# Kernel optimization log

Hardware: AMD Instinct MI355X
Metric: run time of the kernel (lower is better)

## Reference

```python
import jax, jax.numpy as jnp
import numpy as np

B, S = 4, 1800
DA, DP = 438, 72          # audio feat dim, pose dim
DM, NH, DK, DV = 200, 8, 64, 64
DI = 1024                 # ffn inner dim == decoder LSTM hidden
DE = 200                  # pose_emb_size
NL = 2                    # encoder layers
WIN = 100                 # sliding window size
COND, LAMBDA_V = 10, 0.01


def _sinusoid_table(n_pos, d):
    pos = np.arange(n_pos)[:, None].astype(np.float64)
    i = np.arange(d)[None, :]
    ang = pos / np.power(10000.0, 2 * (i // 2) / d)
    t = np.zeros((n_pos, d))
    t[:, 0::2] = np.sin(ang[:, 0::2])
    t[:, 1::2] = np.cos(ang[:, 1::2])
    t[0] = 0.0  # padding_idx
    return jnp.asarray(t, jnp.float32)


def _layer_norm(x, g, b, eps=1e-5):
    m = x.mean(-1, keepdims=True)
    v = ((x - m) ** 2).mean(-1, keepdims=True)
    return (x - m) * jax.lax.rsqrt(v + eps) * g + b


def _lstm_cell(x, h, c, Wih, Whh, bih, bhh):
    g = x @ Wih + h @ Whh + bih + bhh
    i, f, gg, o = jnp.split(g, 4, axis=-1)  # torch gate order i,f,g,o
    c2 = jax.nn.sigmoid(f) * c + jax.nn.sigmoid(i) * jnp.tanh(gg)
    h2 = jax.nn.sigmoid(o) * jnp.tanh(c2)
    return h2, c2


def setup_inputs() -> dict:
    key = jax.random.key(0)
    ks = iter(jax.random.split(key, 64))
    sc = 0.05
    d = {}
    d['src_seq'] = jax.random.normal(next(ks), (B, S, DA), jnp.float32)
    d['tgt_seq'] = jax.random.normal(next(ks), (B, S, DP), jnp.float32)
    d['bos'] = jax.random.normal(next(ks), (B, DP), jnp.float32)
    d['h_init'] = jax.random.normal(next(ks), (3, B, DI), jnp.float32)
    d['c_init'] = jax.random.normal(next(ks), (3, B, DI), jnp.float32)
    d['epoch_i'] = 100
    d['enc_emb_W'] = jax.random.normal(next(ks), (DA, DM)) * sc
    d['enc_emb_b'] = jnp.zeros((DM,))
    d['Wq'] = jax.random.normal(next(ks), (NL, DM, NH * DK)) * sc
    d['bq'] = jnp.zeros((NL, NH * DK))
    d['Wk'] = jax.random.normal(next(ks), (NL, DM, NH * DK)) * sc
    d['bk'] = jnp.zeros((NL, NH * DK))
    d['Wv'] = jax.random.normal(next(ks), (NL, DM, NH * DV)) * sc
    d['bv'] = jnp.zeros((NL, NH * DV))
    d['Wo'] = jax.random.normal(next(ks), (NL, NH * DV, DM)) * sc
    d['bo'] = jnp.zeros((NL, DM))
    d['ln1_g'] = jnp.ones((NL, DM)); d['ln1_b'] = jnp.zeros((NL, DM))
    d['W1'] = jax.random.normal(next(ks), (NL, DM, DI)) * sc
    d['b1'] = jnp.zeros((NL, DI))
    d['W2'] = jax.random.normal(next(ks), (NL, DI, DM)) * sc
    d['b2'] = jnp.zeros((NL, DM))
    d['ln2_g'] = jnp.ones((NL, DM)); d['ln2_b'] = jnp.zeros((NL, DM))
    d['tgt_W'] = jax.random.normal(next(ks), (DP, DE)) * sc
    d['tgt_b'] = jnp.zeros((DE,))
    d['Wih1'] = jax.random.normal(next(ks), (DE, 4 * DI)) * sc
    d['Whh1'] = jax.random.normal(next(ks), (DI, 4 * DI)) * sc
    d['bih1'] = jnp.zeros((4 * DI,)); d['bhh1'] = jnp.zeros((4 * DI,))
    d['Wih2'] = jax.random.normal(next(ks), (DI, 4 * DI)) * sc
    d['Whh2'] = jax.random.normal(next(ks), (DI, 4 * DI)) * sc
    d['bih2'] = jnp.zeros((4 * DI,)); d['bhh2'] = jnp.zeros((4 * DI,))
    d['Wih3'] = jax.random.normal(next(ks), (DI, 4 * DI)) * sc
    d['Whh3'] = jax.random.normal(next(ks), (DI, 4 * DI)) * sc
    d['bih3'] = jnp.zeros((4 * DI,)); d['bhh3'] = jnp.zeros((4 * DI,))
    d['out_W'] = jax.random.normal(next(ks), (DI + DM, DP)) * sc
    d['out_b'] = jnp.zeros((DP,))
    return d


def _forward(src_seq, tgt_seq, bos, h_init, c_init,
             enc_emb_W, enc_emb_b, Wq, bq, Wk, bk, Wv, bv, Wo, bo,
             ln1_g, ln1_b, W1, b1, W2, b2, ln2_g, ln2_b,
             tgt_W, tgt_b, Wih1, Whh1, bih1, bhh1,
             Wih2, Whh2, bih2, bhh2, Wih3, Whh3, bih3, bhh3,
             out_W, out_b, epoch_i):
    # ---------------- Encoder ----------------
    pos = _sinusoid_table(S + 1, DM)[1:S + 1]          # src_pos = arange(S)+1
    x = src_seq @ enc_emb_W + enc_emb_b + pos[None]    # [B,S,DM]
    r = jnp.arange(S)
    keep = jnp.abs(r[:, None] - r[None, :]) <= WIN     # sliding-window band
    for l in range(NL):
        res = x
        q = (x @ Wq[l] + bq[l]).reshape(B, S, NH, DK)
        k = (x @ Wk[l] + bk[l]).reshape(B, S, NH, DK)
        v = (x @ Wv[l] + bv[l]).reshape(B, S, NH, DV)
        att = jnp.einsum('bihd,bjhd->bhij', q, k) / np.sqrt(DK).astype(np.float32)
        att = jnp.where(keep[None, None], att, -1e9)
        att = jax.nn.softmax(att, axis=-1)
        o = jnp.einsum('bhij,bjhd->bihd', att, v).reshape(B, S, NH * DV)
        x = _layer_norm(o @ Wo[l] + bo[l] + res, ln1_g[l], ln1_b[l])
        x = _layer_norm(jax.nn.relu(x @ W1[l] + b1[l]) @ W2[l] + b2[l] + x,
                        ln2_g[l], ln2_b[l])
    enc = x                                            # [B,S,DM]

    # -------- teacher-forcing mask (epoch_i is a Python int) --------
    p = int(epoch_i * LAMBDA_V)
    m = np.concatenate([np.zeros((S, p)), np.ones((S, COND))], 1).reshape(-1)[:S]
    tf_mask = jnp.asarray(m.astype(bool))

    def step(carry, xs):
        h, c, prev = carry                             # h,c: [3,B,DI]
        tgt_t, enc_t, use_gt = xs
        dec_in = jnp.where(use_gt, tgt_t, jax.lax.stop_gradient(prev))
        e = dec_in @ tgt_W + tgt_b
        h0, c0 = _lstm_cell(e,    h[0], c[0], Wih1, Whh1, bih1, bhh1)
        h1, c1 = _lstm_cell(h[0], h[1], c[1], Wih2, Whh2, bih2, bhh2)  # old h0
        h2, c2 = _lstm_cell(h[1], h[2], c[2], Wih3, Whh3, bih3, bhh3)  # old h1
        out = jnp.concatenate([h2, enc_t], -1) @ out_W + out_b
        return (jnp.stack([h0, h1, h2]), jnp.stack([c0, c1, c2]), out), out

    xs = (tgt_seq.transpose(1, 0, 2), enc.transpose(1, 0, 2), tf_mask)
    _, outs = jax.lax.scan(step, (h_init, c_init, bos), xs)
    return outs.transpose(1, 0, 2)                     # [B,S,DP]


def reference(src_seq, tgt_seq, bos, h_init, c_init,
              enc_emb_W, enc_emb_b, Wq, bq, Wk, bk, Wv, bv, Wo, bo,
              ln1_g, ln1_b, W1, b1, W2, b2, ln2_g, ln2_b,
              tgt_W, tgt_b, Wih1, Whh1, bih1, bhh1,
              Wih2, Whh2, bih2, bhh2, Wih3, Whh3, bih3, bhh3,
              out_W, out_b, epoch_i):
    return _forward(src_seq, tgt_seq, bos, h_init, c_init,
                    enc_emb_W, enc_emb_b, Wq, bq, Wk, bk, Wv, bv, Wo, bo,
                    ln1_g, ln1_b, W1, b1, W2, b2, ln2_g, ln2_b,
                    tgt_W, tgt_b, Wih1, Whh1, bih1, bhh1,
                    Wih2, Whh2, bih2, bhh2, Wih3, Whh3, bih3, bhh3,
                    out_W, out_b, epoch_i)
```

## Files before the change

### kernel.cpp

```cpp
#include <hip/hip_runtime.h>

#define SQ 1800
#define NBLK 256

typedef _Float16 h2v __attribute__((ext_vector_type(2)));
#define AGT __HIP_MEMORY_SCOPE_AGENT

__device__ __forceinline__ float bf2f(unsigned short u){ return __uint_as_float(((unsigned)u)<<16); }
__device__ __forceinline__ unsigned short f2bf(float f){
  unsigned u=__float_as_uint(f);
  unsigned r=u+0x7FFFu+((u>>16)&1u);
  return (unsigned short)(r>>16);
}
__device__ __forceinline__ float sigm(float x){ return 1.0f/(1.0f+__expf(-x)); }
__device__ __forceinline__ unsigned pack16(float a, float b){
  _Float16 ha=(_Float16)a, hb=(_Float16)b;
  unsigned short ua=__builtin_bit_cast(unsigned short,ha), ub=__builtin_bit_cast(unsigned short,hb);
  return (unsigned)ua | ((unsigned)ub<<16);
}
__device__ __forceinline__ float lo16(unsigned v){ h2v h=__builtin_bit_cast(h2v,v); return (float)h[0]; }
__device__ __forceinline__ float hi16(unsigned v){ h2v h=__builtin_bit_cast(h2v,v); return (float)h[1]; }
__device__ __forceinline__ float hdot2(unsigned uw, unsigned ux, float acc){
  h2v a=__builtin_bit_cast(h2v,uw), b=__builtin_bit_cast(h2v,ux);
#if __has_builtin(__builtin_amdgcn_fdot2)
  return __builtin_amdgcn_fdot2(a,b,acc,false);
#else
  return acc + (float)a[0]*(float)b[0] + (float)a[1]*(float)b[1];
#endif
}
__device__ __forceinline__ unsigned aload(const unsigned* p){
  return __hip_atomic_load(p,__ATOMIC_RELAXED,AGT);
}
__device__ __forceinline__ unsigned long long aload64(const unsigned long long* p){
  return __hip_atomic_load(p,__ATOMIC_RELAXED,AGT);
}
__device__ __forceinline__ void astore(unsigned* p, unsigned v){
  __hip_atomic_store(p,v,__ATOMIC_RELAXED,AGT);
}


__global__ __launch_bounds__(256) void k_postab(float* __restrict__ pt){
  int idx=blockIdx.x*256+threadIdx.x; if(idx>=SQ*200) return;
  int t=idx/200, j=idx%200;
  double ang=(double)(t+1)*pow(10000.0, -(double)(2*(j/2))/200.0);
  pt[idx]=(float)((j&1)? cos(ang) : sin(ang));
}

__global__ __launch_bounds__(256) void k_we(const float* __restrict__ tgtW, const float* __restrict__ Wih1, float* __restrict__ We){
  int idx=blockIdx.x*256+threadIdx.x;
  int k=idx>>12, j=idx&4095;
  float acc=0.f;
  for(int m=0;m<200;m++) acc+=tgtW[k*200+m]*Wih1[(size_t)m*4096+j];
  We[idx]=acc;
}

__global__ __launch_bounds__(256) void k_bias(const float* __restrict__ tgtb, const float* __restrict__ Wih1,
    const float* __restrict__ bih1,const float* __restrict__ bhh1,const float* __restrict__ bih2,const float* __restrict__ bhh2,
    const float* __restrict__ bih3,const float* __restrict__ bhh3,float* __restrict__ bias){
  int idx=blockIdx.x*256+threadIdx.x; if(idx>=3*4096) return;
  int l=idx>>12, j=idx&4095;
  float v;
  if(l==0){ v=bih1[j]+bhh1[j]; for(int m=0;m<200;m++) v+=tgtb[m]*Wih1[(size_t)m*4096+j]; }
  else if(l==1) v=bih2[j]+bhh2[j];
  else v=bih3[j]+bhh3[j];
  bias[idx]=v;
}

__global__ __launch_bounds__(256) void k_packf(const float* __restrict__ We, const float* __restrict__ Whh1,
  const float* __restrict__ Wih2, const float* __restrict__ Whh2,
  const float* __restrict__ Wih3, const float* __restrict__ Whh3, unsigned* __restrict__ P){
  size_t idx=(size_t)blockIdx.x*256+threadIdx.x;
  const float *A, *Bm; size_t l; int stride, KA, K;
  if(idx < 2359296u){ l=idx; stride=2304; A=We; Bm=Whh1; KA=72; K=1096; }
  else if(idx < 6684672u){ l=idx-2359296u; stride=4224; A=Wih2; Bm=Whh2; KA=1024; K=2048; }
  else { l=idx-6684672u; stride=4224; A=Wih3; Bm=Whh3; KA=1024; K=2048; }
  int u=(int)(l/(size_t)stride); int r=(int)(l-(size_t)u*stride);
  int k2=r>>2, g=r&3, k=2*k2;
  float w0=0.f,w1=0.f;
  if(k<K){
    int col=g*1024+u;
    w0 = (k   < KA)? A[(size_t)k*4096+col]      : Bm[(size_t)(k-KA)*4096+col];
    w1 = (k+1 < KA)? A[(size_t)(k+1)*4096+col]  : Bm[(size_t)(k+1-KA)*4096+col];
  }
  P[idx]=pack16(w0,w1);
}

__global__ __launch_bounds__(256) void k_outwt(const float* __restrict__ outW, float* __restrict__ outWT){
  int idx=blockIdx.x*256+threadIdx.x; if(idx>=72*1024) return;
  int j=idx>>10, u=idx&1023;
  outWT[idx]=outW[(size_t)u*72+j];
}


__global__ __launch_bounds__(256) void k_embed(const float* __restrict__ src, const float* __restrict__ W,
    const float* __restrict__ bias, const float* __restrict__ posb, float* __restrict__ xout){
  __shared__ float s[8][438];
  int row0=blockIdx.x*8, tid=threadIdx.x;
  for(int idx=tid; idx<8*438; idx+=256){ int r=idx/438,k=idx%438; s[r][k]=src[(size_t)(row0+r)*438+k]; }
  __syncthreads();
  int j=tid; if(j<200){
    float acc[8];
    #pragma unroll
    for(int r=0;r<8;r++){ int t=(row0+r)%SQ; acc[r]=bias[j]+posb[t*200+j]; }
    for(int k=0;k<438;k++){
      float w=W[(size_t)k*200+j];
      #pragma unroll
      for(int r=0;r<8;r++) acc[r]+=s[r][k]*w;
    }
    for(int r=0;r<8;r++) xout[(size_t)(row0+r)*200+j]=acc[r];
  }
}

template<int K,int N,int CPT,bool RELU>
__global__ __launch_bounds__(256) void k_gemm8(const float* __restrict__ A, const float* __restrict__ W,
    const float* __restrict__ bias, float* __restrict__ out){
  __shared__ float s[8][K];
  int row0=blockIdx.x*8, tid=threadIdx.x;
  for(int idx=tid; idx<8*K; idx+=256){ int r=idx/K,k=idx%K; s[r][k]=A[(size_t)(row0+r)*K+k]; }
  __syncthreads();
  int j0=tid*CPT;
  float acc[8][CPT];
  #pragma unroll
  for(int r=0;r<8;r++)
    #pragma unroll
    for(int c=0;c<CPT;c++) acc[r][c]=bias[j0+c];
  for(int k=0;k<K;k++){
    float w[CPT];
    #pragma unroll
    for(int c=0;c<CPT;c++) w[c]=W[(size_t)k*N+j0+c];
    #pragma unroll
    for(int r=0;r<8;r++){ float a=s[r][k];
      #pragma unroll
      for(int c=0;c<CPT;c++) acc[r][c]+=a*w[c];
    }
  }
  #pragma unroll
  for(int r=0;r<8;r++)
    #pragma unroll
    for(int c=0;c<CPT;c++){ float v=acc[r][c]; if(RELU) v=fmaxf(v,0.f); out[(size_t)(row0+r)*N+j0+c]=v; }
}

__global__ __launch_bounds__(256) void k_attn(const float* __restrict__ Q, const float* __restrict__ Km,
    const float* __restrict__ V, float* __restrict__ O){
  int bid=blockIdx.x;
  int it=bid%225; int h=(bid/225)&7; int b=bid/1800;
  int i0=it*8;
  int j0=i0-100; if(j0<0) j0=0;
  int j1=i0+7+101; if(j1>SQ) j1=SQ;
  int JN=j1-j0;
  __shared__ unsigned short kld[208][66];
  __shared__ unsigned short vld[208][66];
  __shared__ float q[8][64];
  __shared__ float sc[8][208];
  int tid=threadIdx.x;
  for(int idx=tid; idx<JN*64; idx+=256){
    int j=idx>>6, d=idx&63;
    size_t src=((size_t)(b*SQ+j0+j)*8+h)*64+d;
    kld[j][d]=f2bf(Km[src]);
    vld[j][d]=f2bf(V[src]);
  }
  for(int idx=tid; idx<8*64; idx+=256){ int r=idx>>6,d=idx&63; q[r][d]=Q[((size_t)(b*SQ+i0+r)*8+h)*64+d]; }
  __syncthreads();
  {
    int r=tid>>5, js=tid&31;
    int i=i0+r;
    for(int j=js;j<JN;j+=32){
      int jg=j0+j; int diff=i-jg; if(diff<0) diff=-diff;
      float s=-1e30f;
      if(diff<=100){
        s=0.f;
        for(int d=0;d<64;d++) s+=q[r][d]*bf2f(kld[j][d]);
        s*=0.125f;
      }
      sc[r][j]=s;
    }
  }
  __syncthreads();
  {
    int wv=tid>>6, lane=tid&63;
    for(int rr=wv*2; rr<wv*2+2; rr++){
      float m=-1e30f;
      for(int j=lane;j<JN;j+=64) m=fmaxf(m,sc[rr][j]);
      for(int o=32;o;o>>=1) m=fmaxf(m,__shfl_xor(m,o));
      float sum=0.f;
      for(int j=lane;j<JN;j+=64){ float e=__expf(sc[rr][j]-m); sc[rr][j]=e; sum+=e; }
      for(int o=32;o;o>>=1) sum+=__shfl_xor(sum,o);
      float inv=1.f/sum;
      for(int j=lane;j<JN;j+=64) sc[rr][j]*=inv;
    }
  }
  __syncthreads();
  {
    int d=tid&63, rb=tid>>6;
    for(int rr=rb; rr<8; rr+=4){
      float acc=0.f;
      for(int j=0;j<JN;j++) acc+=sc[rr][j]*bf2f(vld[j][d]);
      O[((size_t)(b*SQ+i0+rr)*8+h)*64+d]=acc;
    }
  }
}

template<int K>
__global__ __launch_bounds__(256) void k_matln(const float* __restrict__ A, const float* __restrict__ W,
    const float* __restrict__ bias, const float* __restrict__ g, const float* __restrict__ bt, float* __restrict__ x){
  __shared__ float s[8][K];
  __shared__ float y[8][200];
  int row0=blockIdx.x*8, tid=threadIdx.x;
  for(int idx=tid; idx<8*K; idx+=256){ int r=idx/K,k=idx%K; s[r][k]=A[(size_t)(row0+r)*K+k]; }
  __syncthreads();
  if(tid<200){
    int j=tid;
    float acc[8];
    #pragma unroll
    for(int r=0;r<8;r++) acc[r]=bias[j];
    for(int k=0;k<K;k++){
      float w=W[(size_t)k*200+j];
      #pragma unroll
      for(int r=0;r<8;r++) acc[r]+=s[r][k]*w;
    }
    #pragma unroll
    for(int r=0;r<8;r++) y[r][j]=acc[r]+x[(size_t)(row0+r)*200+j];
  }
  __syncthreads();
  int wv=tid>>6, lane=tid&63;
  for(int rr=wv*2; rr<wv*2+2; rr++){
    float sm=0.f,s2=0.f;
    for(int j=lane;j<200;j+=64){ float v=y[rr][j]; sm+=v; s2+=v*v; }
    for(int o=32;o;o>>=1){ sm+=__shfl_xor(sm,o); s2+=__shfl_xor(s2,o); }
    float mean=sm*(1.f/200.f);
    float var=s2*(1.f/200.f)-mean*mean;
    float inv=rsqrtf(var+1e-5f);
    for(int j=lane;j<200;j+=64) x[(size_t)(row0+rr)*200+j]=(y[rr][j]-mean)*inv*g[j]+bt[j];
  }
}

__global__ __launch_bounds__(320) void k_encpart(const float* __restrict__ x, const float* __restrict__ outW,
    const float* __restrict__ outb, float* __restrict__ ep){
  int t=blockIdx.x, tid=threadIdx.x;
  __shared__ float el[4][200];
  for(int idx=tid; idx<800; idx+=320){ int b=idx/200,k=idx%200; el[b][k]=x[((size_t)b*SQ+t)*200+k]; }
  __syncthreads();
  if(tid<288){
    int b=tid/72, j=tid%72;
    float acc=outb[j];
    for(int k=0;k<200;k++) acc+=el[b][k]*outW[(size_t)(1024+k)*72+j];
    ep[((size_t)b*SQ+t)*72+j]=acc;
  }
}


__device__ __forceinline__ void gridbar(unsigned* bar, unsigned gen){
  __syncthreads();
  if(threadIdx.x==0){
    int g=blockIdx.x>>4;
    unsigned r=__hip_atomic_fetch_add(&bar[g*32],1u,__ATOMIC_RELAXED,AGT);
    if(r==gen*16u+15u){
      unsigned rt=__hip_atomic_fetch_add(&bar[16*32],1u,__ATOMIC_RELAXED,AGT);
      if(rt==gen*16u+15u){
        __hip_atomic_store(&bar[17*32],gen+1u,__ATOMIC_RELAXED,AGT);
      }
    }
    unsigned f;
    do{ __builtin_amdgcn_s_sleep(1);
        f=__hip_atomic_load(&bar[17*32],__ATOMIC_RELAXED,AGT);
    }while(f<gen+1u);
  }
  __syncthreads();
}

__global__ __launch_bounds__(512,2) void k_dec(
  const uint4* __restrict__ P4, const float* __restrict__ bias,
  unsigned* __restrict__ hbufU, unsigned* __restrict__ fbbufU,
  unsigned* __restrict__ h2allU, unsigned* __restrict__ bar,
  const float* __restrict__ tgt, const float* __restrict__ bos,
  const float* __restrict__ h_init, const float* __restrict__ c_init,
  const float* __restrict__ encp, const float* __restrict__ outWT)
{
  __shared__ __align__(16) unsigned xs2[2688*4];
  __shared__ float red[16*513];
  __shared__ float gsum[192];
  __shared__ float c_lds[48];
  __shared__ float htmp[48];
  __shared__ float ldspad[1200];
  int tid=threadIdx.x, blk=blockIdx.x;
  if(tid==0) ldspad[0]=0.f;

  int uu, ks;
  if(tid<128){ uu=tid>>5; ks=tid&31; }
  else if(tid<320){ int l=tid-128; uu=4+l/48; ks=l-(uu-4)*48; }
  else { int l=tid-320; uu=8+l/48; ks=l-(uu-8)*48; }
  int cell = uu<4?0:(uu<8?1:2);
  int u_loc=uu&3, u_glob=blk*4+u_loc;
  size_t ubase4 = (cell==0)? (size_t)u_glob*576 :
                  (cell==1)? (589824u + (size_t)u_glob*1056) :
                             (1671168u + (size_t)u_glob*1056);
  int xoff = (cell==0)?0:(cell==1?576:1632);

  uint4 w[22];
  if(tid<128){
    #pragma unroll
    for(int i=0;i<18;i++) w[i]=P4[ubase4 + (size_t)ks + (size_t)i*32];
  } else {
    #pragma unroll
    for(int i=0;i<22;i++) w[i]=P4[ubase4 + (size_t)ks + (size_t)i*48];
  }

  int dty[6], dlp[6];
  #pragma unroll
  for(int q=0;q<6;q++){
    int r=tid+512*q; dty[q]=2; dlp[q]=0;
    if(r<2688){
      int cl, rr;
      if(r<576){cl=0;rr=r;} else if(r<1632){cl=1;rr=r-576;} else {cl=2;rr=r-1632;}
      if(cl==0){
        if(rr<36){ dty[q]=1; dlp[q]=2*rr; }
        else if(rr<548){ dty[q]=0; dlp[q]=(0*512+(rr-36))*2; }
      } else {
        int l0=(cl==1)?0:1;
        if(rr<512){ dty[q]=0; dlp[q]=(l0*512+rr)*2; }
        else if(rr<1024){ dty[q]=0; dlp[q]=((l0+1)*512+(rr-512))*2; }
      }
    }
  }

  if(tid<48){
    int uu0=tid>>2, b0=tid&3;
    int cl=uu0<4?0:(uu0<8?1:2);
    c_lds[tid]=c_init[((size_t)cl*4+b0)*1024 + (size_t)blk*4+(uu0&3)];
  }
  __syncthreads();

  const unsigned long long* hb64=(const unsigned long long*)hbufU;
  unsigned gen=0;
  for(int t=0;t<SQ;t++){
    bool fb=(t>0)&&(t%11==0);
    if(fb){
      if(blk<72 && tid<256){
        int j=blk, b=tid>>6, lane=tid&63, pv=(t-1)&1;
        float s=0.f;
        #pragma unroll
        for(int q=0;q<8;q++){
          int u2=lane+q*64;
          unsigned v=aload(&hbufU[(size_t)(((pv*3+2)*512)+u2)*4+b]);
          s += lo16(v)*outWT[(size_t)j*1024+2*u2] + hi16(v)*outWT[(size_t)j*1024+2*u2+1];
        }
        #pragma unroll
        for(int o=32;o;o>>=1) s+=__shfl_xor(s,o);
        if(lane==0) astore(&fbbufU[b*72+j], __float_as_uint(s + encp[((size_t)b*SQ+(t-1))*72+j]));
      }
      gridbar(bar,gen); gen++;
    }

    if(t==0){
      #pragma unroll
      for(int q=0;q<6;q++){
        if(q==5 && tid>=128) break;
        uint4 vv={0u,0u,0u,0u};
        if(dty[q]==1){
          int j=dlp[q];
          const float2 f0=*(const float2*)&bos[0*72+j];
          const float2 f1=*(const float2*)&bos[1*72+j];
          const float2 f2=*(const float2*)&bos[2*72+j];
          const float2 f3=*(const float2*)&bos[3*72+j];
          vv.x=pack16(f0.x,f0.y); vv.y=pack16(f1.x,f1.y);
          vv.z=pack16(f2.x,f2.y); vv.w=pack16(f3.x,f3.y);
        } else if(dty[q]==0){
          int lp=dlp[q]>>10, pr=(dlp[q]>>1)&511;
          const float2 f0=*(const float2*)&h_init[((size_t)lp*4+0)*1024+2*pr];
          const float2 f1=*(const float2*)&h_init[((size_t)lp*4+1)*1024+2*pr];
          const float2 f2=*(const float2*)&h_init[((size_t)lp*4+2)*1024+2*pr];
          const float2 f3=*(const float2*)&h_init[((size_t)lp*4+3)*1024+2*pr];
          vv.x=pack16(f0.x,f0.y); vv.y=pack16(f1.x,f1.y);
          vv.z=pack16(f2.x,f2.y); vv.w=pack16(f3.x,f3.y);
        }
        *(uint4*)&xs2[(size_t)(tid+512*q)*4]=vv;
      }
    } else {
      size_t pvoff=(size_t)(((t-1)&1)*3*512*2);
      #pragma unroll
      for(int q=0;q<6;q++){
        if(q==5 && tid>=128) break;
        int ty=dty[q];
        if(ty==0){
          unsigned long long a=aload64(hb64+pvoff+dlp[q]);
          unsigned long long c=aload64(hb64+pvoff+dlp[q]+1);
          uint4 vv; vv.x=(unsigned)a; vv.y=(unsigned)(a>>32);
          vv.z=(unsigned)c; vv.w=(unsigned)(c>>32);
          *(uint4*)&xs2[(size_t)(tid+512*q)*4]=vv;
        } else if(ty==1){
          int j=dlp[q];
          uint4 vv;
          if(fb){
            vv.x=pack16(__uint_as_float(aload(&fbbufU[0*72+j])),__uint_as_float(aload(&fbbufU[0*72+j+1])));
            vv.y=pack16(__uint_as_float(aload(&fbbufU[1*72+j])),__uint_as_float(aload(&fbbufU[1*72+j+1])));
            vv.z=pack16(__uint_as_float(aload(&fbbufU[2*72+j])),__uint_as_float(aload(&fbbufU[2*72+j+1])));
            vv.w=pack16(__uint_as_float(aload(&fbbufU[3*72+j])),__uint_as_float(aload(&fbbufU[3*72+j+1])));
          } else {
            const float2 f0=*(const float2*)&tgt[((size_t)0*SQ+t)*72+j];
            const float2 f1=*(const float2*)&tgt[((size_t)1*SQ+t)*72+j];
            const float2 f2=*(const float2*)&tgt[((size_t)2*SQ+t)*72+j];
            const float2 f3=*(const float2*)&tgt[((size_t)3*SQ+t)*72+j];
            vv.x=pack16(f0.x,f0.y); vv.y=pack16(f1.x,f1.y);
            vv.z=pack16(f2.x,f2.y); vv.w=pack16(f3.x,f3.y);
          }
          *(uint4*)&xs2[(size_t)(tid+512*q)*4]=vv;
        }
      }
    }
    __syncthreads();

    {
      float acc[16];
      #pragma unroll
      for(int a=0;a<16;a++) acc[a]=0.f;
      auto run=[&](int NIT,int NKS){
        #pragma unroll
        for(int i=0;i<22;i++){
          if(i>=NIT) break;
          const uint4 xv=*(const uint4*)&xs2[(size_t)(xoff+ks+i*NKS)*4];
          const unsigned* wu=(const unsigned*)&w[i];
          const unsigned* xu=(const unsigned*)&xv;
          #pragma unroll
          for(int g=0;g<4;g++)
            #pragma unroll
            for(int b=0;b<4;b++)
              acc[g*4+b]=hdot2(wu[g],xu[b],acc[g*4+b]);
        }
      };
      if(tid<128) run(18,32); else run(22,48);
      #pragma unroll
      for(int a=0;a<16;a++) red[a*513+tid]=acc[a];
    }
    __syncthreads();

    if(tid<192){
      int uuo=tid>>4, a=tid&15;
      int base,n;
      if(uuo<4){base=uuo*32;n=32;} else {base=128+(uuo-4)*48;n=48;}
      float s=0.f;
      for(int j2=0;j2<n;j2++) s+=red[a*513+base+j2];
      int cl=uuo<4?0:(uuo<8?1:2), g=a>>2;
      gsum[tid]=s+bias[(size_t)cl*4096+(size_t)g*1024+blk*4+(uuo&3)];
    }
    __syncthreads();

    if(tid<48){
      int uup=tid>>2,b=tid&3;
      float gi=gsum[uup*16+b],gf=gsum[uup*16+4+b],gg=gsum[uup*16+8+b],go=gsum[uup*16+12+b];
      float cp=c_lds[tid];
      float cn=sigm(gf)*cp+sigm(gi)*tanhf(gg);
      float hn=sigm(go)*tanhf(cn);
      c_lds[tid]=cn; htmp[tid]=hn;
    }
    __syncthreads();
    if(tid<48 && !(tid&4)){
      int uup=tid>>2,b=tid&3;
      int cl=uup<4?0:(uup<8?1:2), ul=uup&3;
      unsigned v=pack16(htmp[tid],htmp[tid+4]);
      int pr=blk*2+(ul>>1);
      astore(&hbufU[(size_t)(((t&1)*3+cl)*512+pr)*4+b], v);
      if(cl==2) astore(&h2allU[((size_t)t*4+b)*512+pr], v);
    }
    gridbar(bar,gen); gen++;
  }
}

__global__ __launch_bounds__(320) void k_out(const unsigned* __restrict__ h2allU, const float* __restrict__ outW,
    const float* __restrict__ enc_part, float* __restrict__ out){
  int t=blockIdx.x, tid=threadIdx.x;
  __shared__ float h2l[4][1024];
  for(int idx=tid; idx<2048; idx+=320){
    int b=idx>>9, p=idx&511;
    unsigned v=h2allU[((size_t)t*4+b)*512+p];
    h2l[b][2*p]=lo16(v); h2l[b][2*p+1]=hi16(v);
  }
  __syncthreads();
  if(tid<288){
    int b=tid/72, j=tid%72;
    float acc=enc_part[((size_t)b*SQ+t)*72+j];
    for(int u=0;u<1024;u++) acc+=h2l[b][u]*outW[(size_t)u*72+j];
    out[((size_t)b*SQ+t)*72+j]=acc;
  }
}

extern "C" void kernel_launch(void* const* d_in, const int* in_sizes, int n_in,
                              void* d_out, int out_size, void* d_ws, size_t ws_size,
                              hipStream_t stream) {
  (void)in_sizes; (void)n_in; (void)out_size; (void)ws_size;
  const float* src   =(const float*)d_in[0];
  const float* tgt   =(const float*)d_in[1];
  const float* bos   =(const float*)d_in[2];
  const float* h_init=(const float*)d_in[3];
  const float* c_init=(const float*)d_in[4];
  const float* eW    =(const float*)d_in[6];
  const float* eb    =(const float*)d_in[7];
  const float* Wq    =(const float*)d_in[8];
  const float* bq    =(const float*)d_in[9];
  const float* Wk    =(const float*)d_in[10];
  const float* bk    =(const float*)d_in[11];
  const float* Wv    =(const float*)d_in[12];
  const float* bv    =(const float*)d_in[13];
  const float* Wo    =(const float*)d_in[14];
  const float* bo    =(const float*)d_in[15];
  const float* ln1g  =(const float*)d_in[16];
  const float* ln1b  =(const float*)d_in[17];
  const float* W1    =(const float*)d_in[18];
  const float* b1    =(const float*)d_in[19];
  const float* W2    =(const float*)d_in[20];
  const float* b2    =(const float*)d_in[21];
  const float* ln2g  =(const float*)d_in[22];
  const float* ln2b  =(const float*)d_in[23];
  const float* tgtW  =(const float*)d_in[24];
  const float* tgtb  =(const float*)d_in[25];
  const float* Wih1  =(const float*)d_in[26];
  const float* Whh1  =(const float*)d_in[27];
  const float* bih1  =(const float*)d_in[28];
  const float* bhh1  =(const float*)d_in[29];
  const float* Wih2  =(const float*)d_in[30];
  const float* Whh2  =(const float*)d_in[31];
  const float* bih2  =(const float*)d_in[32];
  const float* bhh2  =(const float*)d_in[33];
  const float* Wih3  =(const float*)d_in[34];
  const float* Whh3  =(const float*)d_in[35];
  const float* bih3  =(const float*)d_in[36];
  const float* bhh3  =(const float*)d_in[37];
  const float* outW  =(const float*)d_in[38];
  const float* outb  =(const float*)d_in[39];
  float* out=(float*)d_out;

  char* wsb=(char*)d_ws; size_t off=0;
  auto alloc=[&](size_t bytes)->void*{ void* p=wsb+off; off+=(bytes+255)&~(size_t)255; return p; };
  unsigned* Pf   =(unsigned*)alloc((size_t)11010048*4);
  float* We   =(float*)alloc((size_t)72*4096*4);
  float* bias =(float*)alloc((size_t)3*4096*4);
  float* outWT=(float*)alloc((size_t)72*1024*4);
  unsigned* hbufU =(unsigned*)alloc((size_t)2*3*512*4*4);
  unsigned* fbbufU=(unsigned*)alloc((size_t)4*72*4);
  unsigned* bar   =(unsigned*)alloc(4096);
  float* encp =(float*)alloc((size_t)7200*72*4);
  float* posb =(float*)alloc((size_t)SQ*200*4);
  float* xb   =(float*)alloc((size_t)7200*200*4);
  float* qb   =(float*)alloc((size_t)7200*512*4);
  float* kb   =(float*)alloc((size_t)7200*512*4);
  float* vb   =(float*)alloc((size_t)7200*512*4);
  float* ob   =(float*)alloc((size_t)7200*512*4);
  unsigned* h2allU=(unsigned*)qb;
  float* mid  =vb;
  (void)kb; (void)ob;

  k_postab<<<(SQ*200+255)/256,256,0,stream>>>(posb);
  k_we<<<72*4096/256,256,0,stream>>>(tgtW,Wih1,We);
  k_bias<<<48,256,0,stream>>>(tgtb,Wih1,bih1,bhh1,bih2,bhh2,bih3,bhh3,bias);
  k_packf<<<43008,256,0,stream>>>(We,Whh1,Wih2,Whh2,Wih3,Whh3,Pf);
  k_outwt<<<(72*1024+255)/256,256,0,stream>>>(outW,outWT);

  k_embed<<<900,256,0,stream>>>(src,eW,eb,posb,xb);
  for(int l=0;l<2;l++){
    k_gemm8<200,512,2,false><<<900,256,0,stream>>>(xb,Wq+(size_t)l*200*512,bq+l*512,qb);
    k_gemm8<200,512,2,false><<<900,256,0,stream>>>(xb,Wk+(size_t)l*200*512,bk+l*512,kb);
    k_gemm8<200,512,2,false><<<900,256,0,stream>>>(xb,Wv+(size_t)l*200*512,bv+l*512,vb);
    k_attn<<<7200,256,0,stream>>>(qb,kb,vb,ob);
    k_matln<512><<<900,256,0,stream>>>(ob,Wo+(size_t)l*512*200,bo+l*200,ln1g+l*200,ln1b+l*200,xb);
    k_gemm8<200,1024,4,true><<<900,256,0,stream>>>(xb,W1+(size_t)l*200*1024,b1+l*1024,mid);
    k_matln<1024><<<900,256,0,stream>>>(mid,W2+(size_t)l*1024*200,b2+l*200,ln2g+l*200,ln2b+l*200,xb);
  }
  k_encpart<<<SQ,320,0,stream>>>(xb,outW,outb,encp);

  hipMemsetAsync(bar,0,4096,stream);
  k_dec<<<NBLK,512,0,stream>>>((const uint4*)Pf,bias,hbufU,fbbufU,h2allU,bar,
                               tgt,bos,h_init,c_init,encp,outWT);

  k_out<<<SQ,320,0,stream>>>(h2allU,outW,encp,out);
}
```

Measured before the change: 14.74 ms.

## Split decoder LSTM into two pipelined block groups with point-to-point flags

The persistent decoder kernel is split into two groups of 128 blocks. Group A computes LSTM layers 1 and 2 and group B computes layer 3, so layer 3 of step t can overlap with layers 1 and 2 of the next step. The single all-block grid barrier is replaced by per-group barriers plus cross-group progress counters, and the hidden-state ring buffer grows from 2 to 4 slots to allow the lag. Weight packing strides change to match the new per-thread k-split. The risk is more complex synchronisation and a possible imbalance between the two groups.

```diff
diff --git a/kernel.cpp b/kernel.cpp
--- a/kernel.cpp
+++ b/kernel.cpp
@@ -72,8 +72,8 @@
   size_t idx=(size_t)blockIdx.x*256+threadIdx.x;
   const float *A, *Bm; size_t l; int stride, KA, K;
   if(idx < 2359296u){ l=idx; stride=2304; A=We; Bm=Whh1; KA=72; K=1096; }
-  else if(idx < 6684672u){ l=idx-2359296u; stride=4224; A=Wih2; Bm=Whh2; KA=1024; K=2048; }
-  else { l=idx-6684672u; stride=4224; A=Wih3; Bm=Whh3; KA=1024; K=2048; }
+  else if(idx < 6782976u){ l=idx-2359296u; stride=4320; A=Wih2; Bm=Whh2; KA=1024; K=2048; }
+  else { l=idx-6782976u; stride=4352; A=Wih3; Bm=Whh3; KA=1024; K=2048; }
   int u=(int)(l/(size_t)stride); int r=(int)(l-(size_t)u*stride);
   int k2=r>>2, g=r&3, k=2*k2;
   float w0=0.f,w1=0.f;
@@ -249,25 +249,6 @@
 }
 
 
-__device__ __forceinline__ void gridbar(unsigned* bar, unsigned gen){
-  __syncthreads();
-  if(threadIdx.x==0){
-    int g=blockIdx.x>>4;
-    unsigned r=__hip_atomic_fetch_add(&bar[g*32],1u,__ATOMIC_RELAXED,AGT);
-    if(r==gen*16u+15u){
-      unsigned rt=__hip_atomic_fetch_add(&bar[16*32],1u,__ATOMIC_RELAXED,AGT);
-      if(rt==gen*16u+15u){
-        __hip_atomic_store(&bar[17*32],gen+1u,__ATOMIC_RELAXED,AGT);
-      }
-    }
-    unsigned f;
-    do{ __builtin_amdgcn_s_sleep(1);
-        f=__hip_atomic_load(&bar[17*32],__ATOMIC_RELAXED,AGT);
-    }while(f<gen+1u);
-  }
-  __syncthreads();
-}
-
 __global__ __launch_bounds__(512,2) void k_dec(
   const uint4* __restrict__ P4, const float* __restrict__ bias,
   unsigned* __restrict__ hbufU, unsigned* __restrict__ fbbufU,
@@ -276,87 +257,93 @@
   const float* __restrict__ h_init, const float* __restrict__ c_init,
   const float* __restrict__ encp, const float* __restrict__ outWT)
 {
-  __shared__ __align__(16) unsigned xs2[2688*4];
+  __shared__ __align__(16) unsigned xs2[1116*4];
   __shared__ float red[16*513];
-  __shared__ float gsum[192];
-  __shared__ float c_lds[48];
-  __shared__ float htmp[48];
-  __shared__ float ldspad[1200];
+  __shared__ float gsum[256];
+  __shared__ float c_lds[64];
+  __shared__ float htmp[64];
+  __shared__ float ldspad[8192];
   int tid=threadIdx.x, blk=blockIdx.x;
+  bool isA = blk<128;
+  int lblk = isA? blk : blk-128;
   if(tid==0) ldspad[0]=0.f;
 
-  int uu, ks;
-  if(tid<128){ uu=tid>>5; ks=tid&31; }
-  else if(tid<320){ int l=tid-128; uu=4+l/48; ks=l-(uu-4)*48; }
-  else { int l=tid-320; uu=8+l/48; ks=l-(uu-8)*48; }
-  int cell = uu<4?0:(uu<8?1:2);
-  int u_loc=uu&3, u_glob=blk*4+u_loc;
-  size_t ubase4 = (cell==0)? (size_t)u_glob*576 :
-                  (cell==1)? (589824u + (size_t)u_glob*1056) :
-                             (1671168u + (size_t)u_glob*1056);
-  int xoff = (cell==0)?0:(cell==1?576:1632);
-
-  uint4 w[22];
-  if(tid<128){
-    #pragma unroll
-    for(int i=0;i<18;i++) w[i]=P4[ubase4 + (size_t)ks + (size_t)i*32];
-  } else {
-    #pragma unroll
-    for(int i=0;i<22;i++) w[i]=P4[ubase4 + (size_t)ks + (size_t)i*48];
-  }
-
-  int dty[6], dlp[6];
+  int slot,ks,NKS,NIT,xoff,cell;
+  if(isA){
+    if(tid<192){ slot=tid/24; ks=tid-slot*24; NKS=24; NIT=24; xoff=0; cell=0; }
+    else { int l=tid-192; slot=8+l/40; ks=l-(slot-8)*40; NKS=40; NIT=27; xoff=36; cell=1; }
+  } else { slot=tid>>6; ks=tid&63; NKS=64; NIT=17; xoff=0; cell=2; }
+  int unit = lblk*8 + (slot&7);
+  size_t ubase4 = (cell==0)? (size_t)unit*576 :
+                  (cell==1)? (589824u + (size_t)unit*1080) :
+                             (1695744u + (size_t)unit*1088);
+
+  uint4 w[27];
   #pragma unroll
-  for(int q=0;q<6;q++){
-    int r=tid+512*q; dty[q]=2; dlp[q]=0;
-    if(r<2688){
-      int cl, rr;
-      if(r<576){cl=0;rr=r;} else if(r<1632){cl=1;rr=r-576;} else {cl=2;rr=r-1632;}
-      if(cl==0){
-        if(rr<36){ dty[q]=1; dlp[q]=2*rr; }
-        else if(rr<548){ dty[q]=0; dlp[q]=(0*512+(rr-36))*2; }
-      } else {
-        int l0=(cl==1)?0:1;
-        if(rr<512){ dty[q]=0; dlp[q]=(l0*512+rr)*2; }
-        else if(rr<1024){ dty[q]=0; dlp[q]=((l0+1)*512+(rr-512))*2; }
-      }
-    }
-  }
-
-  if(tid<48){
-    int uu0=tid>>2, b0=tid&3;
-    int cl=uu0<4?0:(uu0<8?1:2);
-    c_lds[tid]=c_init[((size_t)cl*4+b0)*1024 + (size_t)blk*4+(uu0&3)];
-  }
+  for(int i=0;i<27;i++){ if(i<NIT) w[i]=P4[ubase4 + (size_t)ks + (size_t)i*NKS]; }
+
+  int dty[3], dlp[3];
+  #pragma unroll
+  for(int q=0;q<3;q++){
+    int r=tid+512*q; dty[q]=3; dlp[q]=0;
+    if(isA){
+      if(r<36){ dty[q]=1; dlp[q]=2*r; }
+      else if(r<548){ dty[q]=0; dlp[q]=(r-36)*2; }
+      else if(r<1060){ dty[q]=0; dlp[q]=(512+(r-548))*2; }
+      else if(r<1116){ dty[q]=2; }
+    } else {
+      if(r<512){ dty[q]=0; dlp[q]=(512+r)*2; }
+      else if(r<1024){ dty[q]=0; dlp[q]=(1024+(r-512))*2; }
+      else if(r<1088){ dty[q]=2; }
+    }
+  }
+
+  if(isA){ if(tid<64){ int s=tid>>2,b=tid&3; int cl=(s<8)?0:1;
+           c_lds[tid]=c_init[((size_t)cl*4+b)*1024 + lblk*8+(s&7)]; } }
+  else   { if(tid<32){ int s=tid>>2,b=tid&3;
+           c_lds[tid]=c_init[((size_t)2*4+b)*1024 + lblk*8+s]; } }
   __syncthreads();
 
   const unsigned long long* hb64=(const unsigned long long*)hbufU;
   unsigned gen=0;
   for(int t=0;t<SQ;t++){
     bool fb=(t>0)&&(t%11==0);
-    if(fb){
-      if(blk<72 && tid<256){
-        int j=blk, b=tid>>6, lane=tid&63, pv=(t-1)&1;
+
+    if(!isA && fb){
+      if(lblk<72 && tid<256){
+        int j=lblk, b=tid>>6, lane=tid&63, sl=(t-1)&3;
         float s=0.f;
         #pragma unroll
         for(int q=0;q<8;q++){
           int u2=lane+q*64;
-          unsigned v=aload(&hbufU[(size_t)(((pv*3+2)*512)+u2)*4+b]);
+          unsigned v=aload(&hbufU[(size_t)((sl*3+2)*512+u2)*4+b]);
           s += lo16(v)*outWT[(size_t)j*1024+2*u2] + hi16(v)*outWT[(size_t)j*1024+2*u2+1];
         }
         #pragma unroll
         for(int o=32;o;o>>=1) s+=__shfl_xor(s,o);
         if(lane==0) astore(&fbbufU[b*72+j], __float_as_uint(s + encp[((size_t)b*SQ+(t-1))*72+j]));
       }
-      gridbar(bar,gen); gen++;
+      __syncthreads();
+      if(tid==0 && lblk<72) __hip_atomic_fetch_add(&bar[640],1u,__ATOMIC_RELAXED,AGT);
+    }
+
+    if(isA){
+      if(tid<64){
+        if(t>=2){ while((int)aload(&bar[608]) < t-2) __builtin_amdgcn_s_sleep(1); }
+        if(fb){ unsigned tc=72u*(unsigned)(t/11);
+                while(aload(&bar[640]) < tc) __builtin_amdgcn_s_sleep(1); }
+      }
+    } else if(t>0){
+      if(tid<64){ while((int)aload(&bar[576]) < t) __builtin_amdgcn_s_sleep(1); }
+      __syncthreads();
     }
 
     if(t==0){
       #pragma unroll
-      for(int q=0;q<6;q++){
-        if(q==5 && tid>=128) break;
+      for(int q=0;q<3;q++){
+        int ty=dty[q]; if(ty==3) continue;
         uint4 vv={0u,0u,0u,0u};
-        if(dty[q]==1){
+        if(ty==1){
           int j=dlp[q];
           const float2 f0=*(const float2*)&bos[0*72+j];
           const float2 f1=*(const float2*)&bos[1*72+j];
@@ -364,8 +351,8 @@
           const float2 f3=*(const float2*)&bos[3*72+j];
           vv.x=pack16(f0.x,f0.y); vv.y=pack16(f1.x,f1.y);
           vv.z=pack16(f2.x,f2.y); vv.w=pack16(f3.x,f3.y);
-        } else if(dty[q]==0){
-          int lp=dlp[q]>>10, pr=(dlp[q]>>1)&511;
+        } else if(ty==0){
+          int lp=dlp[q]>>10, pr=(dlp[q]&1023)>>1;
           const float2 f0=*(const float2*)&h_init[((size_t)lp*4+0)*1024+2*pr];
           const float2 f1=*(const float2*)&h_init[((size_t)lp*4+1)*1024+2*pr];
           const float2 f2=*(const float2*)&h_init[((size_t)lp*4+2)*1024+2*pr];
@@ -376,20 +363,18 @@
         *(uint4*)&xs2[(size_t)(tid+512*q)*4]=vv;
       }
     } else {
-      size_t pvoff=(size_t)(((t-1)&1)*3*512*2);
-      #pragma unroll
-      for(int q=0;q<6;q++){
-        if(q==5 && tid>=128) break;
-        int ty=dty[q];
+      size_t pvoff=(size_t)(((t-1)&3)*3*512*2);
+      #pragma unroll
+      for(int q=0;q<3;q++){
+        int ty=dty[q]; if(ty>=2) continue;
+        uint4 vv;
         if(ty==0){
           unsigned long long a=aload64(hb64+pvoff+dlp[q]);
           unsigned long long c=aload64(hb64+pvoff+dlp[q]+1);
-          uint4 vv; vv.x=(unsigned)a; vv.y=(unsigned)(a>>32);
+          vv.x=(unsigned)a; vv.y=(unsigned)(a>>32);
           vv.z=(unsigned)c; vv.w=(unsigned)(c>>32);
-          *(uint4*)&xs2[(size_t)(tid+512*q)*4]=vv;
-        } else if(ty==1){
+        } else {
           int j=dlp[q];
-          uint4 vv;
           if(fb){
             vv.x=pack16(__uint_as_float(aload(&fbbufU[0*72+j])),__uint_as_float(aload(&fbbufU[0*72+j+1])));
             vv.y=pack16(__uint_as_float(aload(&fbbufU[1*72+j])),__uint_as_float(aload(&fbbufU[1*72+j+1])));
@@ -403,8 +388,8 @@
             vv.x=pack16(f0.x,f0.y); vv.y=pack16(f1.x,f1.y);
             vv.z=pack16(f2.x,f2.y); vv.w=pack16(f3.x,f3.y);
           }
-          *(uint4*)&xs2[(size_t)(tid+512*q)*4]=vv;
         }
+        *(uint4*)&xs2[(size_t)(tid+512*q)*4]=vv;
       }
     }
     __syncthreads();
@@ -413,55 +398,90 @@
       float acc[16];
       #pragma unroll
       for(int a=0;a<16;a++) acc[a]=0.f;
-      auto run=[&](int NIT,int NKS){
+      #pragma unroll
+      for(int i=0;i<27;i++){
+        if(i>=NIT) break;
+        const uint4 xv=*(const uint4*)&xs2[(size_t)(xoff+ks+i*NKS)*4];
+        const unsigned* wu=(const unsigned*)&w[i];
+        const unsigned* xu=(const unsigned*)&xv;
         #pragma unroll
-        for(int i=0;i<22;i++){
-          if(i>=NIT) break;
-          const uint4 xv=*(const uint4*)&xs2[(size_t)(xoff+ks+i*NKS)*4];
-          const unsigned* wu=(const unsigned*)&w[i];
-          const unsigned* xu=(const unsigned*)&xv;
+        for(int g=0;g<4;g++)
           #pragma unroll
-          for(int g=0;g<4;g++)
-            #pragma unroll
-            for(int b=0;b<4;b++)
-              acc[g*4+b]=hdot2(wu[g],xu[b],acc[g*4+b]);
+          for(int b=0;b<4;b++)
+            acc[g*4+b]=hdot2(wu[g],xu[b],acc[g*4+b]);
+      }
+      #pragma unroll
+      for(int a=0;a<16;a++) red[a*513+tid]=acc[a];
+    }
+    __syncthreads();
+
+    if(isA){
+      if(tid<256){
+        int s=tid>>4, a=tid&15;
+        int base = (s<8)? s*24 : 192+(s-8)*40;
+        int n = (s<8)? 24 : 40;
+        float sum=0.f;
+        for(int j2=0;j2<n;j2++) sum+=red[a*513+base+j2];
+        int cl=(s<8)?0:1;
+        gsum[tid]=sum+bias[(size_t)cl*4096+(size_t)(a>>2)*1024 + lblk*8+(s&7)];
+      }
+    } else {
+      if(tid<128){
+        int s=tid>>4, a=tid&15;
+        float sum=0.f;
+        for(int j2=0;j2<64;j2++) sum+=red[a*513+s*64+j2];
+        gsum[tid]=sum+bias[(size_t)2*4096+(size_t)(a>>2)*1024 + lblk*8+s];
+      }
+    }
+    __syncthreads();
+
+    if(isA){
+      if(tid<64){
+        int s=tid>>2,b=tid&3;
+        float gi=gsum[s*16+b],gf=gsum[s*16+4+b],gg=gsum[s*16+8+b],go=gsum[s*16+12+b];
+        float cp=c_lds[tid];
+        float cn=sigm(gf)*cp+sigm(gi)*tanhf(gg);
+        float hn=sigm(go)*tanhf(cn);
+        c_lds[tid]=cn; htmp[tid]=hn;
+        if(!(tid&4)){
+          unsigned v=pack16(htmp[tid],htmp[tid+4]);
+          int layer=s>>3, sl=s&7;
+          int pr=lblk*4+(sl>>1);
+          astore(&hbufU[(size_t)(((t&3)*3+layer)*512+pr)*4+b], v);
         }
-      };
-      if(tid<128) run(18,32); else run(22,48);
-      #pragma unroll
-      for(int a=0;a<16;a++) red[a*513+tid]=acc[a];
-    }
+      }
+    } else {
+      if(tid<32){
+        int s=tid>>2,b=tid&3;
+        float gi=gsum[s*16+b],gf=gsum[s*16+4+b],gg=gsum[s*16+8+b],go=gsum[s*16+12+b];
+        float cp=c_lds[tid];
+        float cn=sigm(gf)*cp+sigm(gi)*tanhf(gg);
+        float hn=sigm(go)*tanhf(cn);
+        c_lds[tid]=cn; htmp[tid]=hn;
+        if(!(tid&4)){
+          unsigned v=pack16(htmp[tid],htmp[tid+4]);
+          int pr=lblk*4+(s>>1);
+          astore(&hbufU[(size_t)(((t&3)*3+2)*512+pr)*4+b], v);
+          astore(&h2allU[((size_t)t*4+b)*512+pr], v);
+        }
+      }
+    }
+
     __syncthreads();
-
-    if(tid<192){
-      int uuo=tid>>4, a=tid&15;
-      int base,n;
-      if(uuo<4){base=uuo*32;n=32;} else {base=128+(uuo-4)*48;n=48;}
-      float s=0.f;
-      for(int j2=0;j2<n;j2++) s+=red[a*513+base+j2];
-      int cl=uuo<4?0:(uuo<8?1:2), g=a>>2;
-      gsum[tid]=s+bias[(size_t)cl*4096+(size_t)g*1024+blk*4+(uuo&3)];
+    if(tid==0){
+      int g=blk>>4;
+      unsigned r=__hip_atomic_fetch_add(&bar[g*32],1u,__ATOMIC_RELAXED,AGT);
+      if(r==gen*16u+15u){
+        unsigned rt=__hip_atomic_fetch_add(&bar[isA?512:544],1u,__ATOMIC_RELAXED,AGT);
+        if(rt==gen*8u+7u) __hip_atomic_store(&bar[isA?576:608],gen+1u,__ATOMIC_RELAXED,AGT);
+      }
+      unsigned f;
+      do{ __builtin_amdgcn_s_sleep(1);
+          f=aload(&bar[isA?576:608]);
+      }while(f<gen+1u);
     }
     __syncthreads();
-
-    if(tid<48){
-      int uup=tid>>2,b=tid&3;
-      float gi=gsum[uup*16+b],gf=gsum[uup*16+4+b],gg=gsum[uup*16+8+b],go=gsum[uup*16+12+b];
-      float cp=c_lds[tid];
-      float cn=sigm(gf)*cp+sigm(gi)*tanhf(gg);
-      float hn=sigm(go)*tanhf(cn);
-      c_lds[tid]=cn; htmp[tid]=hn;
-    }
-    __syncthreads();
-    if(tid<48 && !(tid&4)){
-      int uup=tid>>2,b=tid&3;
-      int cl=uup<4?0:(uup<8?1:2), ul=uup&3;
-      unsigned v=pack16(htmp[tid],htmp[tid+4]);
-      int pr=blk*2+(ul>>1);
-      astore(&hbufU[(size_t)(((t&1)*3+cl)*512+pr)*4+b], v);
-      if(cl==2) astore(&h2allU[((size_t)t*4+b)*512+pr], v);
-    }
-    gridbar(bar,gen); gen++;
+    gen++;
   }
 }
 
@@ -530,11 +550,11 @@
 
   char* wsb=(char*)d_ws; size_t off=0;
   auto alloc=[&](size_t bytes)->void*{ void* p=wsb+off; off+=(bytes+255)&~(size_t)255; return p; };
-  unsigned* Pf   =(unsigned*)alloc((size_t)11010048*4);
+  unsigned* Pf   =(unsigned*)alloc((size_t)11239424*4);
   float* We   =(float*)alloc((size_t)72*4096*4);
   float* bias =(float*)alloc((size_t)3*4096*4);
   float* outWT=(float*)alloc((size_t)72*1024*4);
-  unsigned* hbufU =(unsigned*)alloc((size_t)2*3*512*4*4);
+  unsigned* hbufU =(unsigned*)alloc((size_t)4*3*512*4*4);
   unsigned* fbbufU=(unsigned*)alloc((size_t)4*72*4);
   unsigned* bar   =(unsigned*)alloc(4096);
   float* encp =(float*)alloc((size_t)7200*72*4);
@@ -551,7 +571,7 @@
   k_postab<<<(SQ*200+255)/256,256,0,stream>>>(posb);
   k_we<<<72*4096/256,256,0,stream>>>(tgtW,Wih1,We);
   k_bias<<<48,256,0,stream>>>(tgtb,Wih1,bih1,bhh1,bih2,bhh2,bih3,bhh3,bias);
-  k_packf<<<43008,256,0,stream>>>(We,Whh1,Wih2,Whh2,Wih3,Whh3,Pf);
+  k_packf<<<43904,256,0,stream>>>(We,Whh1,Wih2,Whh2,Wih3,Whh3,Pf);
   k_outwt<<<(72*1024+255)/256,256,0,stream>>>(outW,outWT);
 
   k_embed<<<900,256,0,stream>>>(src,eW,eb,posb,xb);
```

New measurement: 26.87 ms. +82.3%, slower.
